# Kernel optimization log

Measured on AMD Instinct MI355X. Metric: run time of the kernel, lower is better.

The kernel has to match this reference:

```python
import jax, jax.numpy as jnp
import numpy as np

N_NODES = 100000
N_EDGES = 1600000
IN_CH, HID_CH, OUT_CH = 128, 64, 40


def setup_inputs() -> dict:
    key = jax.random.key(0)
    k_x, k_e, k_w1, k_w2 = jax.random.split(key, 4)
    x = jax.random.normal(k_x, (N_NODES, IN_CH), dtype=jnp.float32)
    edge_index = jax.random.randint(k_e, (2, N_EDGES), 0, N_NODES, dtype=jnp.int64)
    # Glorot-ish scaled weights, zero bias (matches GCNConv init convention)
    W1 = jax.random.normal(k_w1, (IN_CH, HID_CH), dtype=jnp.float32) / np.sqrt(IN_CH)
    b1 = jnp.zeros((HID_CH,), dtype=jnp.float32)
    W2 = jax.random.normal(k_w2, (HID_CH, OUT_CH), dtype=jnp.float32) / np.sqrt(HID_CH)
    b2 = jnp.zeros((OUT_CH,), dtype=jnp.float32)
    return {"x": x, "edge_index": edge_index, "W1": W1, "b1": b1, "W2": W2, "b2": b2}


def _gcn_conv(x, edge_index, W, b, n):
    """GCNConv with normalize=True: linear transform, add self-loops,
    symmetric D^-1/2 A D^-1/2 aggregation (source_to_target flow), bias."""
    h = x @ W  # [n, out]
    loops = jnp.arange(n, dtype=edge_index.dtype)
    row = jnp.concatenate([edge_index[0], loops])  # sources
    col = jnp.concatenate([edge_index[1], loops])  # targets
    deg = jax.ops.segment_sum(jnp.ones_like(col, dtype=h.dtype), col, num_segments=n)
    dinv = jnp.where(deg > 0, jax.lax.rsqrt(deg), jnp.zeros_like(deg))
    w = dinv[row] * dinv[col]  # [E+n] per-edge norm
    out = jax.ops.segment_sum(h[row] * w[:, None], col, num_segments=n)  # scatter-add to targets
    return out + b


def reference(x, edge_index, W1, b1, W2, b2):
    # eval mode: F.dropout(p=0.8, training=False) is identity
    n = x.shape[0]
    h = jax.nn.relu(_gcn_conv(x, edge_index, W1, b1, n))
    return _gcn_conv(h, edge_index, W2, b2, n)  # [N, OUT_CH] logits
```

## Files before the change

kernel.cpp:

```cpp
#include <hip/hip_runtime.h>

#define N_NODES 100000
#define N_EDGES 1600000
#define IN_CH   128
#define HID_CH  64
#define OUT_CH  40
#define NBKT    196
#define EPB     4096
#define CAP     9216

using bf16x8 = __attribute__((ext_vector_type(8))) short;
using f32x4  = __attribute__((ext_vector_type(4))) float;

__device__ __forceinline__ float bf2f(unsigned short u) {
    union { unsigned int i; float f; } c; c.i = ((unsigned int)u) << 16; return c.f;
}
__device__ __forceinline__ unsigned short f2bf(float f) {
    union { float f; unsigned int i; } c; c.f = f;
    unsigned int r = c.i + 0x7FFFu + ((c.i >> 16) & 1u);
    return (unsigned short)(r >> 16);
}
__device__ __forceinline__ float4 bf2f4(ushort4 u) {
    return make_float4(bf2f(u.x), bf2f(u.y), bf2f(u.z), bf2f(u.w));
}

__global__ void k_bin(const int* __restrict__ ei, int* __restrict__ gcur,
                      int* __restrict__ ebuf) {
    __shared__ int hist[NBKT];
    __shared__ int lcur[NBKT];
    int tid = threadIdx.x;
    int base = blockIdx.x * EPB;
    int nloc = N_EDGES - base;
    if (nloc > EPB) nloc = EPB;
    int n4 = nloc >> 2;
    const int4* S4 = (const int4*)(ei + base);
    const int4* D4 = (const int4*)(ei + N_EDGES + base);

    if (tid < NBKT) { hist[tid] = 0; }
    __syncthreads();
    for (int i = tid; i < n4; i += 256) {
        int4 d = D4[i];
        atomicAdd(&hist[d.x >> 9], 1);
        atomicAdd(&hist[d.y >> 9], 1);
        atomicAdd(&hist[d.z >> 9], 1);
        atomicAdd(&hist[d.w >> 9], 1);
    }
    __syncthreads();
    if (tid < NBKT) {
        int h = hist[tid];
        lcur[tid] = h ? (tid * CAP + atomicAdd(&gcur[tid], h)) : 0;
    }
    __syncthreads();
    for (int i = tid; i < n4; i += 256) {
        int4 s = S4[i];
        int4 d = D4[i];
        int p;
        p = atomicAdd(&lcur[d.x >> 9], 1); ebuf[p] = s.x | ((d.x & 511) << 17);
        p = atomicAdd(&lcur[d.y >> 9], 1); ebuf[p] = s.y | ((d.y & 511) << 17);
        p = atomicAdd(&lcur[d.z >> 9], 1); ebuf[p] = s.z | ((d.z & 511) << 17);
        p = atomicAdd(&lcur[d.w >> 9], 1); ebuf[p] = s.w | ((d.w & 511) << 17);
    }
}

__global__ void k_node(const int* __restrict__ gcur, const int* __restrict__ ebuf,
                       int* __restrict__ row_start, int* __restrict__ row_end,
                       int* __restrict__ csr_src, float* __restrict__ dinv) {
    __shared__ int cnt[512];
    __shared__ int s[512];
    int tid = threadIdx.x;
    int b = blockIdx.x;
    int node0 = b << 9;
    int lo = b * CAP;
    int hi = lo + gcur[b];
    int n = hi - lo, n4 = n >> 2;
    const int4* E4 = (const int4*)(ebuf + lo);

    cnt[tid] = 0;
    __syncthreads();
    for (int i = tid; i < n4; i += 512) {
        int4 w = E4[i];
        atomicAdd(&cnt[(unsigned)w.x >> 17], 1);
        atomicAdd(&cnt[(unsigned)w.y >> 17], 1);
        atomicAdd(&cnt[(unsigned)w.z >> 17], 1);
        atomicAdd(&cnt[(unsigned)w.w >> 17], 1);
    }
    for (int e = lo + (n4 << 2) + tid; e < hi; e += 512)
        atomicAdd(&cnt[(unsigned)ebuf[e] >> 17], 1);
    __syncthreads();
    int c = cnt[tid];
    s[tid] = c;
    __syncthreads();
#pragma unroll
    for (int off = 1; off < 512; off <<= 1) {
        int tv = (tid >= off) ? s[tid - off] : 0;
        __syncthreads();
        s[tid] += tv;
        __syncthreads();
    }
    int node = node0 + tid;
    if (node < N_NODES) {
        row_start[node] = lo + s[tid] - c;
        row_end[node]   = lo + s[tid];
        dinv[node] = rsqrtf(1.0f + (float)c);
    }
    __syncthreads();
    cnt[tid] = lo + s[tid] - c;
    __syncthreads();
    for (int i = tid; i < n4; i += 512) {
        int4 w = E4[i];
        int p;
        p = atomicAdd(&cnt[(unsigned)w.x >> 17], 1); csr_src[p] = w.x & 0x1FFFF;
        p = atomicAdd(&cnt[(unsigned)w.y >> 17], 1); csr_src[p] = w.y & 0x1FFFF;
        p = atomicAdd(&cnt[(unsigned)w.z >> 17], 1); csr_src[p] = w.z & 0x1FFFF;
        p = atomicAdd(&cnt[(unsigned)w.w >> 17], 1); csr_src[p] = w.w & 0x1FFFF;
    }
    for (int e = lo + (n4 << 2) + tid; e < hi; e += 512) {
        int w = ebuf[e];
        int p = atomicAdd(&cnt[(unsigned)w >> 17], 1);
        csr_src[p] = w & 0x1FFFF;
    }
}

__global__ __launch_bounds__(256, 4)
void k_gemm1(const float* __restrict__ x, const float* __restrict__ W1,
             const float* __restrict__ dinv, unsigned short* __restrict__ h1s) {
    __shared__ unsigned short Al[64 * 136];
    __shared__ unsigned short Bl[64 * 136];
    __shared__ float dl[64];
    int tid = threadIdx.x;
    long long node0 = (long long)blockIdx.x * 64;

    const float4* X = (const float4*)x;
    for (int i = tid; i < 64 * 32; i += 256) {
        int r = i >> 5, c4 = i & 31;
        long long gr = node0 + r;
        if (gr >= N_NODES) gr = N_NODES - 1;
        float4 v = X[gr * 32 + c4];
        *(ushort4*)&Al[r * 136 + c4 * 4] =
            make_ushort4(f2bf(v.x), f2bf(v.y), f2bf(v.z), f2bf(v.w));
    }
    for (int i = tid; i < 128 * 64; i += 256) {
        int k = i >> 6, nn = i & 63;
        Bl[nn * 136 + k] = f2bf(W1[i]);
    }
    if (tid < 64) {
        long long gr = node0 + tid;
        dl[tid] = dinv[gr < N_NODES ? gr : N_NODES - 1];
    }
    __syncthreads();

    int lane = tid & 63, wave = tid >> 6;
    int quad = lane >> 4, l16 = lane & 15;
    int arow = wave * 16 + l16;
    f32x4 ac0 = {0,0,0,0}, ac1 = {0,0,0,0}, ac2 = {0,0,0,0}, ac3 = {0,0,0,0};

#pragma unroll
    for (int ks = 0; ks < 4; ++ks) {
        int ko = ks * 32 + quad * 8;
        bf16x8 a  = *(const bf16x8*)&Al[arow * 136 + ko];
        bf16x8 b0 = *(const bf16x8*)&Bl[( 0 + l16) * 136 + ko];
        bf16x8 b1 = *(const bf16x8*)&Bl[(16 + l16) * 136 + ko];
        bf16x8 b2 = *(const bf16x8*)&Bl[(32 + l16) * 136 + ko];
        bf16x8 b3 = *(const bf16x8*)&Bl[(48 + l16) * 136 + ko];
        ac0 = __builtin_amdgcn_mfma_f32_16x16x32_bf16(a, b0, ac0, 0, 0, 0);
        ac1 = __builtin_amdgcn_mfma_f32_16x16x32_bf16(a, b1, ac1, 0, 0, 0);
        ac2 = __builtin_amdgcn_mfma_f32_16x16x32_bf16(a, b2, ac2, 0, 0, 0);
        ac3 = __builtin_amdgcn_mfma_f32_16x16x32_bf16(a, b3, ac3, 0, 0, 0);
    }

#pragma unroll
    for (int r = 0; r < 4; ++r) {
        int rl = wave * 16 + quad * 4 + r;
        long long grow = node0 + rl;
        if (grow < N_NODES) {
            float dd = dl[rl];
            h1s[grow * 64 +  0 + l16] = f2bf(ac0[r] * dd);
            h1s[grow * 64 + 16 + l16] = f2bf(ac1[r] * dd);
            h1s[grow * 64 + 32 + l16] = f2bf(ac2[r] * dd);
            h1s[grow * 64 + 48 + l16] = f2bf(ac3[r] * dd);
        }
    }
}

__global__ __launch_bounds__(256, 4)
void k_agg1g2(const int* __restrict__ row_start, const int* __restrict__ row_end,
              const int* __restrict__ csr_src,
              const unsigned short* __restrict__ h1s, const float* __restrict__ dinv,
              const float* __restrict__ b1, const float* __restrict__ W2,
              unsigned short* __restrict__ h2s) {
    __shared__ unsigned short Al[64 * 72];
    __shared__ unsigned short Bl[48 * 72];
    __shared__ float dl[64];
    int tid = threadIdx.x;
    long long node0 = (long long)blockIdx.x * 64;

    for (int i = tid; i < 48 * 64; i += 256) {
        int nn = i >> 6, k = i & 63;
        Bl[nn * 72 + k] = f2bf(nn < OUT_CH ? W2[k * OUT_CH + nn] : 0.0f);
    }
    if (tid < 64) {
        long long gr = node0 + tid;
        dl[tid] = dinv[gr < N_NODES ? gr : N_NODES - 1];
    }
    __syncthreads();

    int cg = tid & 15;
    int nsub = tid >> 4;
    float4 bb = ((const float4*)b1)[cg];
    const ushort4* H = (const ushort4*)h1s;

#pragma unroll
    for (int r4 = 0; r4 < 4; ++r4) {
        int nl = r4 * 16 + nsub;
        long long node = node0 + nl;
        ushort4 res = make_ushort4(0, 0, 0, 0);
        if (node < N_NODES) {
            int e = row_start[node];
            int nd = row_end[node] - e;
            float4 a0 = bf2f4(H[node * 16 + cg]);
            float4 a1 = {0.f,0.f,0.f,0.f}, a2 = {0.f,0.f,0.f,0.f}, a3 = {0.f,0.f,0.f,0.f};
            while (nd > 0) {
                int kk = cg < nd ? cg : nd - 1;
                int idxr = csr_src[e + kk];
                int K = nd < 16 ? nd : 16;
#define GSTEP(J, A) { int ss = __shfl(idxr, J, 16); \
                      ushort4 rw = H[(long long)ss * 16 + cg]; \
                      if (J < K) { float4 v = bf2f4(rw); \
                        A.x += v.x; A.y += v.y; A.z += v.z; A.w += v.w; } }
                GSTEP( 0, a0) GSTEP( 1, a1) GSTEP( 2, a2) GSTEP( 3, a3)
                GSTEP( 4, a0) GSTEP( 5, a1) GSTEP( 6, a2) GSTEP( 7, a3)
                GSTEP( 8, a0) GSTEP( 9, a1) GSTEP(10, a2) GSTEP(11, a3)
                GSTEP(12, a0) GSTEP(13, a1) GSTEP(14, a2) GSTEP(15, a3)
#undef GSTEP
                e += 16; nd -= 16;
            }
            a0.x += a1.x + a2.x + a3.x;
            a0.y += a1.y + a2.y + a3.y;
            a0.z += a1.z + a2.z + a3.z;
            a0.w += a1.w + a2.w + a3.w;
            float dd = dl[nl];
            res = make_ushort4(f2bf(fmaxf(a0.x * dd + bb.x, 0.f)),
                               f2bf(fmaxf(a0.y * dd + bb.y, 0.f)),
                               f2bf(fmaxf(a0.z * dd + bb.z, 0.f)),
                               f2bf(fmaxf(a0.w * dd + bb.w, 0.f)));
        }
        *(ushort4*)&Al[nl * 72 + cg * 4] = res;
    }
    __syncthreads();

    int lane = tid & 63, wave = tid >> 6;
    int quad = lane >> 4, l16 = lane & 15;
    int arow = wave * 16 + l16;
    f32x4 ac0 = {0,0,0,0}, ac1 = {0,0,0,0}, ac2 = {0,0,0,0};

#pragma unroll
    for (int ks = 0; ks < 2; ++ks) {
        int ko = ks * 32 + quad * 8;
        bf16x8 a  = *(const bf16x8*)&Al[arow * 72 + ko];
        bf16x8 b0 = *(const bf16x8*)&Bl[( 0 + l16) * 72 + ko];
        bf16x8 b1v = *(const bf16x8*)&Bl[(16 + l16) * 72 + ko];
        bf16x8 b2 = *(const bf16x8*)&Bl[(32 + l16) * 72 + ko];
        ac0 = __builtin_amdgcn_mfma_f32_16x16x32_bf16(a, b0, ac0, 0, 0, 0);
        ac1 = __builtin_amdgcn_mfma_f32_16x16x32_bf16(a, b1v, ac1, 0, 0, 0);
        ac2 = __builtin_amdgcn_mfma_f32_16x16x32_bf16(a, b2, ac2, 0, 0, 0);
    }

#pragma unroll
    for (int r = 0; r < 4; ++r) {
        int rl = wave * 16 + quad * 4 + r;
        long long grow = node0 + rl;
        if (grow < N_NODES) {
            float dd = dl[rl];
            h2s[grow * 40 +  0 + l16] = f2bf(ac0[r] * dd);
            h2s[grow * 40 + 16 + l16] = f2bf(ac1[r] * dd);
            if (l16 < 8) h2s[grow * 40 + 32 + l16] = f2bf(ac2[r] * dd);
        }
    }
}

__global__ __launch_bounds__(256, 4)
void k_agg2(const int* __restrict__ row_start, const int* __restrict__ row_end,
            const int* __restrict__ csr_src,
            const unsigned short* __restrict__ h2s, const float* __restrict__ dinv,
            const float* __restrict__ b2, float* __restrict__ out) {
    int idx = blockIdx.x * blockDim.x + threadIdx.x;
    int node = idx >> 4;
    int cg = idx & 15;
    if (node >= N_NODES) return;
    int e = row_start[node];
    int nd = row_end[node] - e;
    const ushort4* H = (const ushort4*)h2s;
    bool act = cg < 10;
    float4 a0 = {0.f,0.f,0.f,0.f}, a1 = a0, a2 = a0, a3 = a0;
    if (act) a0 = bf2f4(H[(long long)node * 10 + cg]);
    while (nd > 0) {
        int kk = cg < nd ? cg : nd - 1;
        int idxr = csr_src[e + kk];
        int K = nd < 16 ? nd : 16;
#define GSTEP2(J, A) { int ss = __shfl(idxr, J, 16); \
                       if (act && J < K) { \
                         float4 v = bf2f4(H[(long long)ss * 10 + cg]); \
                         A.x += v.x; A.y += v.y; A.z += v.z; A.w += v.w; } }
        GSTEP2( 0, a0) GSTEP2( 1, a1) GSTEP2( 2, a2) GSTEP2( 3, a3)
        GSTEP2( 4, a0) GSTEP2( 5, a1) GSTEP2( 6, a2) GSTEP2( 7, a3)
        GSTEP2( 8, a0) GSTEP2( 9, a1) GSTEP2(10, a2) GSTEP2(11, a3)
        GSTEP2(12, a0) GSTEP2(13, a1) GSTEP2(14, a2) GSTEP2(15, a3)
#undef GSTEP2
        e += 16; nd -= 16;
    }
    if (act) {
        a0.x += a1.x + a2.x + a3.x;
        a0.y += a1.y + a2.y + a3.y;
        a0.z += a1.z + a2.z + a3.z;
        a0.w += a1.w + a2.w + a3.w;
        float dd = dinv[node];
        float4 b = ((const float4*)b2)[cg];
        a0.x = a0.x * dd + b.x;
        a0.y = a0.y * dd + b.y;
        a0.z = a0.z * dd + b.z;
        a0.w = a0.w * dd + b.w;
        ((float4*)out)[(long long)node * 10 + cg] = a0;
    }
}

extern "C" void kernel_launch(void* const* d_in, const int* in_sizes, int n_in,
                              void* d_out, int out_size, void* d_ws, size_t ws_size,
                              hipStream_t stream) {
    const float* x  = (const float*)d_in[0];
    const int*   ei = (const int*)d_in[1];
    const float* W1 = (const float*)d_in[2];
    const float* b1 = (const float*)d_in[3];
    const float* W2 = (const float*)d_in[4];
    const float* b2 = (const float*)d_in[5];
    float* out = (float*)d_out;

    unsigned short* hbuf  = (unsigned short*)d_ws;
    unsigned short* h2buf = hbuf + 64LL * N_NODES;
    int* ebuf      = (int*)(h2buf + 64LL * N_NODES);
    int* csr_src   = ebuf + NBKT * CAP;
    int* row_start = csr_src + NBKT * CAP;
    int* row_end   = row_start + N_NODES;
    int* gcur      = row_end + N_NODES;
    float* dinv    = (float*)(gcur + 256);

    const int B = 256;
    const int g16 = (N_NODES * 16 + B - 1) / B;
    const int gRows = (N_NODES + 63) / 64;

    hipMemsetAsync((void*)gcur, 0, NBKT * sizeof(int), stream);
    k_bin<<<(N_EDGES + EPB - 1) / EPB, B, 0, stream>>>(ei, gcur, ebuf);
    k_node<<<NBKT, 512, 0, stream>>>(gcur, ebuf, row_start, row_end, csr_src, dinv);

    k_gemm1<<<gRows, B, 0, stream>>>(x, W1, dinv, hbuf);
    k_agg1g2<<<gRows, B, 0, stream>>>(row_start, row_end, csr_src, hbuf, dinv,
                                      b1, W2, h2buf);
    k_agg2<<<g16, B, 0, stream>>>(row_start, row_end, csr_src, h2buf, dinv, b2, out);
}
```

Baseline: 236.6 us.

## Switch aggregation to edge-balanced merge-path with packed CSR and LDS atomics

Both aggregation kernels now split a 64-node block's contiguous edge range evenly across 16 lane groups instead of giving each group one node. Each CSR entry carries its local destination packed in the high bits, so a group can run-length accumulate per destination and flush partial sums to a shared-memory accumulator with atomics. The aim is to remove load imbalance and the wasted masked gather slots on low-degree nodes, and to issue all 16 gathers before consuming them. The cost is LDS atomic traffic at segment boundaries, extra shared memory that may lower occupancy, and a separate epilogue pass.

```diff
diff --git a/kernel.cpp b/kernel.cpp
--- a/kernel.cpp
+++ b/kernel.cpp
@@ -64,7 +64,7 @@
 
 __global__ void k_node(const int* __restrict__ gcur, const int* __restrict__ ebuf,
                        int* __restrict__ row_start, int* __restrict__ row_end,
-                       int* __restrict__ csr_src, float* __restrict__ dinv) {
+                       int* __restrict__ csr_pk, float* __restrict__ dinv) {
     __shared__ int cnt[512];
     __shared__ int s[512];
     int tid = threadIdx.x;
@@ -109,15 +109,15 @@
     for (int i = tid; i < n4; i += 512) {
         int4 w = E4[i];
         int p;
-        p = atomicAdd(&cnt[(unsigned)w.x >> 17], 1); csr_src[p] = w.x & 0x1FFFF;
-        p = atomicAdd(&cnt[(unsigned)w.y >> 17], 1); csr_src[p] = w.y & 0x1FFFF;
-        p = atomicAdd(&cnt[(unsigned)w.z >> 17], 1); csr_src[p] = w.z & 0x1FFFF;
-        p = atomicAdd(&cnt[(unsigned)w.w >> 17], 1); csr_src[p] = w.w & 0x1FFFF;
+        p = atomicAdd(&cnt[(unsigned)w.x >> 17], 1); csr_pk[p] = w.x;
+        p = atomicAdd(&cnt[(unsigned)w.y >> 17], 1); csr_pk[p] = w.y;
+        p = atomicAdd(&cnt[(unsigned)w.z >> 17], 1); csr_pk[p] = w.z;
+        p = atomicAdd(&cnt[(unsigned)w.w >> 17], 1); csr_pk[p] = w.w;
     }
     for (int e = lo + (n4 << 2) + tid; e < hi; e += 512) {
         int w = ebuf[e];
         int p = atomicAdd(&cnt[(unsigned)w >> 17], 1);
-        csr_src[p] = w & 0x1FFFF;
+        csr_pk[p] = w;
     }
 }
 
@@ -184,67 +184,92 @@
 
 __global__ __launch_bounds__(256, 4)
 void k_agg1g2(const int* __restrict__ row_start, const int* __restrict__ row_end,
-              const int* __restrict__ csr_src,
+              const int* __restrict__ csr_pk,
               const unsigned short* __restrict__ h1s, const float* __restrict__ dinv,
               const float* __restrict__ b1, const float* __restrict__ W2,
               unsigned short* __restrict__ h2s) {
+    __shared__ float accL[64 * 68];
     __shared__ unsigned short Al[64 * 72];
     __shared__ unsigned short Bl[48 * 72];
     __shared__ float dl[64];
     int tid = threadIdx.x;
-    long long node0 = (long long)blockIdx.x * 64;
+    int node0 = blockIdx.x * 64;
+    int blocal = node0 & 511;
 
     for (int i = tid; i < 48 * 64; i += 256) {
         int nn = i >> 6, k = i & 63;
         Bl[nn * 72 + k] = f2bf(nn < OUT_CH ? W2[k * OUT_CH + nn] : 0.0f);
     }
     if (tid < 64) {
-        long long gr = node0 + tid;
+        int gr = node0 + tid;
         dl[tid] = dinv[gr < N_NODES ? gr : N_NODES - 1];
     }
-    __syncthreads();
-
-    int cg = tid & 15;
-    int nsub = tid >> 4;
-    float4 bb = ((const float4*)b1)[cg];
+    for (int i = tid; i < 64 * 68; i += 256) accL[i] = 0.0f;
+    __syncthreads();
+
+    int g = tid >> 4, cg = tid & 15;
+    int e0 = row_start[node0];
+    int lastn = node0 + 63; if (lastn >= N_NODES) lastn = N_NODES - 1;
+    int e1 = row_end[lastn];
+    int L = e1 - e0;
+    int e   = e0 + (int)(((long long)L * g) >> 4);
+    int end = e0 + (int)(((long long)L * (g + 1)) >> 4);
+
     const ushort4* H = (const ushort4*)h1s;
-
-#pragma unroll
-    for (int r4 = 0; r4 < 4; ++r4) {
-        int nl = r4 * 16 + nsub;
-        long long node = node0 + nl;
-        ushort4 res = make_ushort4(0, 0, 0, 0);
-        if (node < N_NODES) {
-            int e = row_start[node];
-            int nd = row_end[node] - e;
-            float4 a0 = bf2f4(H[node * 16 + cg]);
-            float4 a1 = {0.f,0.f,0.f,0.f}, a2 = {0.f,0.f,0.f,0.f}, a3 = {0.f,0.f,0.f,0.f};
-            while (nd > 0) {
-                int kk = cg < nd ? cg : nd - 1;
-                int idxr = csr_src[e + kk];
-                int K = nd < 16 ? nd : 16;
-#define GSTEP(J, A) { int ss = __shfl(idxr, J, 16); \
-                      ushort4 rw = H[(long long)ss * 16 + cg]; \
-                      if (J < K) { float4 v = bf2f4(rw); \
-                        A.x += v.x; A.y += v.y; A.z += v.z; A.w += v.w; } }
-                GSTEP( 0, a0) GSTEP( 1, a1) GSTEP( 2, a2) GSTEP( 3, a3)
-                GSTEP( 4, a0) GSTEP( 5, a1) GSTEP( 6, a2) GSTEP( 7, a3)
-                GSTEP( 8, a0) GSTEP( 9, a1) GSTEP(10, a2) GSTEP(11, a3)
-                GSTEP(12, a0) GSTEP(13, a1) GSTEP(14, a2) GSTEP(15, a3)
-#undef GSTEP
-                e += 16; nd -= 16;
+    float4 ar = {0.f, 0.f, 0.f, 0.f};
+    int cur = -1;
+
+#define FLUSH1 { int nl_ = cur - blocal; float* A_ = &accL[nl_ * 68 + cg * 4]; \
+    atomicAdd(A_ + 0, ar.x); atomicAdd(A_ + 1, ar.y); \
+    atomicAdd(A_ + 2, ar.z); atomicAdd(A_ + 3, ar.w); }
+#define LD1(J)  int w##J = __shfl(pk, J, 16); \
+    ushort4 v##J = H[(long long)(w##J & 0x1FFFF) * 16 + cg];
+#define LD1T(J) int w##J = __shfl(pk, J, 16); \
+    ushort4 v##J = make_ushort4(0,0,0,0); \
+    if (J < rem) v##J = H[(long long)(w##J & 0x1FFFF) * 16 + cg];
+#define PR1(J) { int d_ = (unsigned)w##J >> 17; float4 t_ = bf2f4(v##J); \
+    if (d_ != cur) { if (cur >= 0) FLUSH1; cur = d_; ar = t_; } \
+    else { ar.x += t_.x; ar.y += t_.y; ar.z += t_.z; ar.w += t_.w; } }
+#define PR1T(J) if (J < rem) PR1(J)
+
+    while (e + 16 <= end) {
+        int pk = csr_pk[e + cg];
+        LD1(0)  LD1(1)  LD1(2)  LD1(3)  LD1(4)  LD1(5)  LD1(6)  LD1(7)
+        LD1(8)  LD1(9)  LD1(10) LD1(11) LD1(12) LD1(13) LD1(14) LD1(15)
+        PR1(0)  PR1(1)  PR1(2)  PR1(3)  PR1(4)  PR1(5)  PR1(6)  PR1(7)
+        PR1(8)  PR1(9)  PR1(10) PR1(11) PR1(12) PR1(13) PR1(14) PR1(15)
+        e += 16;
+    }
+    int rem = end - e;
+    if (rem > 0) {
+        int pk = csr_pk[e + (cg < rem ? cg : rem - 1)];
+        LD1T(0)  LD1T(1)  LD1T(2)  LD1T(3)  LD1T(4)  LD1T(5)  LD1T(6)  LD1T(7)
+        LD1T(8)  LD1T(9)  LD1T(10) LD1T(11) LD1T(12) LD1T(13) LD1T(14) LD1T(15)
+        PR1T(0)  PR1T(1)  PR1T(2)  PR1T(3)  PR1T(4)  PR1T(5)  PR1T(6)  PR1T(7)
+        PR1T(8)  PR1T(9)  PR1T(10) PR1T(11) PR1T(12) PR1T(13) PR1T(14) PR1T(15)
+    }
+    if (cur >= 0) FLUSH1;
+#undef FLUSH1
+#undef LD1
+#undef LD1T
+#undef PR1
+#undef PR1T
+    __syncthreads();
+
+    {
+        int ch = tid & 63;
+        float b1c = b1[ch];
+        for (int i = tid; i < 64 * 64; i += 256) {
+            int nl = i >> 6;
+            int node = node0 + nl;
+            unsigned short r = 0;
+            if (node < N_NODES) {
+                float val = accL[nl * 68 + ch]
+                          + bf2f(h1s[(long long)node * 64 + ch]);
+                r = f2bf(fmaxf(val * dl[nl] + b1c, 0.f));
             }
-            a0.x += a1.x + a2.x + a3.x;
-            a0.y += a1.y + a2.y + a3.y;
-            a0.z += a1.z + a2.z + a3.z;
-            a0.w += a1.w + a2.w + a3.w;
-            float dd = dl[nl];
-            res = make_ushort4(f2bf(fmaxf(a0.x * dd + bb.x, 0.f)),
-                               f2bf(fmaxf(a0.y * dd + bb.y, 0.f)),
-                               f2bf(fmaxf(a0.z * dd + bb.z, 0.f)),
-                               f2bf(fmaxf(a0.w * dd + bb.w, 0.f)));
+            Al[nl * 72 + ch] = r;
         }
-        *(ushort4*)&Al[nl * 72 + cg * 4] = res;
     }
     __syncthreads();
 
@@ -280,46 +305,85 @@
 
 __global__ __launch_bounds__(256, 4)
 void k_agg2(const int* __restrict__ row_start, const int* __restrict__ row_end,
-            const int* __restrict__ csr_src,
+            const int* __restrict__ csr_pk,
             const unsigned short* __restrict__ h2s, const float* __restrict__ dinv,
             const float* __restrict__ b2, float* __restrict__ out) {
-    int idx = blockIdx.x * blockDim.x + threadIdx.x;
-    int node = idx >> 4;
-    int cg = idx & 15;
-    if (node >= N_NODES) return;
-    int e = row_start[node];
-    int nd = row_end[node] - e;
+    __shared__ float acc2[64 * 44];
+    int tid = threadIdx.x;
+    int node0 = blockIdx.x * 64;
+    int blocal = node0 & 511;
+
+    for (int i = tid; i < 64 * 44; i += 256) acc2[i] = 0.0f;
+    __syncthreads();
+
+    int g = tid >> 4, cg = tid & 15;
+    bool act = cg < 10;
+    int e0 = row_start[node0];
+    int lastn = node0 + 63; if (lastn >= N_NODES) lastn = N_NODES - 1;
+    int e1 = row_end[lastn];
+    int L = e1 - e0;
+    int e   = e0 + (int)(((long long)L * g) >> 4);
+    int end = e0 + (int)(((long long)L * (g + 1)) >> 4);
+
     const ushort4* H = (const ushort4*)h2s;
-    bool act = cg < 10;
-    float4 a0 = {0.f,0.f,0.f,0.f}, a1 = a0, a2 = a0, a3 = a0;
-    if (act) a0 = bf2f4(H[(long long)node * 10 + cg]);
-    while (nd > 0) {
-        int kk = cg < nd ? cg : nd - 1;
-        int idxr = csr_src[e + kk];
-        int K = nd < 16 ? nd : 16;
-#define GSTEP2(J, A) { int ss = __shfl(idxr, J, 16); \
-                       if (act && J < K) { \
-                         float4 v = bf2f4(H[(long long)ss * 10 + cg]); \
-                         A.x += v.x; A.y += v.y; A.z += v.z; A.w += v.w; } }
-        GSTEP2( 0, a0) GSTEP2( 1, a1) GSTEP2( 2, a2) GSTEP2( 3, a3)
-        GSTEP2( 4, a0) GSTEP2( 5, a1) GSTEP2( 6, a2) GSTEP2( 7, a3)
-        GSTEP2( 8, a0) GSTEP2( 9, a1) GSTEP2(10, a2) GSTEP2(11, a3)
-        GSTEP2(12, a0) GSTEP2(13, a1) GSTEP2(14, a2) GSTEP2(15, a3)
-#undef GSTEP2
-        e += 16; nd -= 16;
-    }
-    if (act) {
-        a0.x += a1.x + a2.x + a3.x;
-        a0.y += a1.y + a2.y + a3.y;
-        a0.z += a1.z + a2.z + a3.z;
-        a0.w += a1.w + a2.w + a3.w;
+    float4 ar = {0.f, 0.f, 0.f, 0.f};
+    int cur = -1;
+
+#define FLUSH2 { int nl_ = cur - blocal; float* A_ = &acc2[nl_ * 44 + cg * 4]; \
+    atomicAdd(A_ + 0, ar.x); atomicAdd(A_ + 1, ar.y); \
+    atomicAdd(A_ + 2, ar.z); atomicAdd(A_ + 3, ar.w); }
+#define LD2(J)  int w##J = __shfl(pk, J, 16); \
+    ushort4 v##J = make_ushort4(0,0,0,0); \
+    if (act) v##J = H[(long long)(w##J & 0x1FFFF) * 10 + cg];
+#define LD2T(J) int w##J = __shfl(pk, J, 16); \
+    ushort4 v##J = make_ushort4(0,0,0,0); \
+    if (act && J < rem) v##J = H[(long long)(w##J & 0x1FFFF) * 10 + cg];
+#define PR2(J) { int d_ = (unsigned)w##J >> 17; float4 t_ = bf2f4(v##J); \
+    if (d_ != cur) { if (cur >= 0 && act) FLUSH2; cur = d_; ar = t_; } \
+    else { ar.x += t_.x; ar.y += t_.y; ar.z += t_.z; ar.w += t_.w; } }
+#define PR2T(J) if (J < rem) PR2(J)
+
+    while (e + 16 <= end) {
+        int pk = csr_pk[e + cg];
+        LD2(0)  LD2(1)  LD2(2)  LD2(3)  LD2(4)  LD2(5)  LD2(6)  LD2(7)
+        LD2(8)  LD2(9)  LD2(10) LD2(11) LD2(12) LD2(13) LD2(14) LD2(15)
+        PR2(0)  PR2(1)  PR2(2)  PR2(3)  PR2(4)  PR2(5)  PR2(6)  PR2(7)
+        PR2(8)  PR2(9)  PR2(10) PR2(11) PR2(12) PR2(13) PR2(14) PR2(15)
+        e += 16;
+    }
+    int rem = end - e;
+    if (rem > 0) {
+        int pk = csr_pk[e + (cg < rem ? cg : rem - 1)];
+        LD2T(0)  LD2T(1)  LD2T(2)  LD2T(3)  LD2T(4)  LD2T(5)  LD2T(6)  LD2T(7)
+        LD2T(8)  LD2T(9)  LD2T(10) LD2T(11) LD2T(12) LD2T(13) LD2T(14) LD2T(15)
+        PR2T(0)  PR2T(1)  PR2T(2)  PR2T(3)  PR2T(4)  PR2T(5)  PR2T(6)  PR2T(7)
+        PR2T(8)  PR2T(9)  PR2T(10) PR2T(11) PR2T(12) PR2T(13) PR2T(14) PR2T(15)
+    }
+    if (cur >= 0 && act) FLUSH2;
+#undef FLUSH2
+#undef LD2
+#undef LD2T
+#undef PR2
+#undef PR2T
+    __syncthreads();
+
+    for (int i = tid; i < 64 * 10; i += 256) {
+        int nl = i / 10, c = i % 10;
+        int node = node0 + nl;
+        if (node >= N_NODES) break;
+        float4 v;
+        v.x = acc2[nl * 44 + c * 4 + 0];
+        v.y = acc2[nl * 44 + c * 4 + 1];
+        v.z = acc2[nl * 44 + c * 4 + 2];
+        v.w = acc2[nl * 44 + c * 4 + 3];
+        float4 sf = bf2f4(H[(long long)node * 10 + c]);
         float dd = dinv[node];
-        float4 b = ((const float4*)b2)[cg];
-        a0.x = a0.x * dd + b.x;
-        a0.y = a0.y * dd + b.y;
-        a0.z = a0.z * dd + b.z;
-        a0.w = a0.w * dd + b.w;
-        ((float4*)out)[(long long)node * 10 + cg] = a0;
+        float4 b = ((const float4*)b2)[c];
+        v.x = (v.x + sf.x) * dd + b.x;
+        v.y = (v.y + sf.y) * dd + b.y;
+        v.z = (v.z + sf.z) * dd + b.z;
+        v.w = (v.w + sf.w) * dd + b.w;
+        ((float4*)out)[(long long)node * 10 + c] = v;
     }
 }
 
@@ -337,22 +401,21 @@
     unsigned short* hbuf  = (unsigned short*)d_ws;
     unsigned short* h2buf = hbuf + 64LL * N_NODES;
     int* ebuf      = (int*)(h2buf + 64LL * N_NODES);
-    int* csr_src   = ebuf + NBKT * CAP;
-    int* row_start = csr_src + NBKT * CAP;
+    int* csr_pk    = ebuf + NBKT * CAP;
+    int* row_start = csr_pk + NBKT * CAP;
     int* row_end   = row_start + N_NODES;
     int* gcur      = row_end + N_NODES;
     float* dinv    = (float*)(gcur + 256);
 
     const int B = 256;
-    const int g16 = (N_NODES * 16 + B - 1) / B;
     const int gRows = (N_NODES + 63) / 64;
 
     hipMemsetAsync((void*)gcur, 0, NBKT * sizeof(int), stream);
     k_bin<<<(N_EDGES + EPB - 1) / EPB, B, 0, stream>>>(ei, gcur, ebuf);
-    k_node<<<NBKT, 512, 0, stream>>>(gcur, ebuf, row_start, row_end, csr_src, dinv);
+    k_node<<<NBKT, 512, 0, stream>>>(gcur, ebuf, row_start, row_end, csr_pk, dinv);
 
     k_gemm1<<<gRows, B, 0, stream>>>(x, W1, dinv, hbuf);
-    k_agg1g2<<<gRows, B, 0, stream>>>(row_start, row_end, csr_src, hbuf, dinv,
+    k_agg1g2<<<gRows, B, 0, stream>>>(row_start, row_end, csr_pk, hbuf, dinv,
                                       b1, W2, h2buf);
-    k_agg2<<<g16, B, 0, stream>>>(row_start, row_end, csr_src, h2buf, dinv, b2, out);
-}
+    k_agg2<<<gRows, B, 0, stream>>>(row_start, row_end, csr_pk, h2buf, dinv, b2, out);
+}
```

Result: slower. 262.6 us (+11.0%).
